# Optimization experiments

Hardware: AMD Instinct MI355X
Metric: run time of the kernel (lower is better)

Reference implementation:

```python
import jax, jax.numpy as jnp
import numpy as np


def _gru_cell(h, x, Wih, Whh, bih, bhh):
    # PyTorch GRU cell, gate order (r, z, n)
    gi = x @ Wih.T + bih      # [B, 3H]
    gh = h @ Whh.T + bhh      # [B, 3H]
    i_r, i_z, i_n = jnp.split(gi, 3, axis=-1)
    h_r, h_z, h_n = jnp.split(gh, 3, axis=-1)
    r = jax.nn.sigmoid(i_r + h_r)
    z = jax.nn.sigmoid(i_z + h_z)
    n = jnp.tanh(i_n + r * h_n)
    return (1.0 - z) * n + z * h


def _run_gru(xs, h0, Wih, Whh, bih, bhh):
    # xs: [T, B, E] -> (h_T [B, H], outputs [T, B, H])
    def step(h, x):
        h = _gru_cell(h, x, Wih, Whh, bih, bhh)
        return h, h
    return jax.lax.scan(step, h0, xs)


def setup_inputs() -> dict:
    key = jax.random.key(0)
    ks = jax.random.split(key, 14)
    V, E, H1, H2, W, C = 101, 512, 1024, 1024, 2048, 24

    def p(k, shape, fan):
        return jax.random.normal(k, shape, jnp.float32) / np.float32(np.sqrt(fan))

    return {
        "x": jax.random.randint(ks[0], (1, W, C), 0, V),
        "emb": p(ks[1], (V, E), E),
        "Wih1": p(ks[2], (3 * H1, E), E),
        "Whh1": p(ks[3], (3 * H1, H1), H1),
        "bih1": jnp.zeros((3 * H1,), jnp.float32),
        "bhh1": jnp.zeros((3 * H1,), jnp.float32),
        "Wih2f": p(ks[4], (3 * H2, H1), H1),
        "Whh2f": p(ks[5], (3 * H2, H2), H2),
        "bih2f": jnp.zeros((3 * H2,), jnp.float32),
        "bhh2f": jnp.zeros((3 * H2,), jnp.float32),
        "Wih2b": p(ks[6], (3 * H2, H1), H1),
        "Whh2b": p(ks[7], (3 * H2, H2), H2),
        "bih2b": jnp.zeros((3 * H2,), jnp.float32),
        "bhh2b": jnp.zeros((3 * H2,), jnp.float32),
    }


def reference(x, emb, Wih1, Whh1, bih1, bhh1,
              Wih2f, Whh2f, bih2f, bhh2f,
              Wih2b, Whh2b, bih2b, bhh2b):
    # x: [1, W, C] int indices. Dropout is treated as eval-mode (identity).
    Wn = x.shape[1]
    H1 = Whh1.shape[1]
    H2 = Whh2f.shape[1]

    e = emb[x[0]]                       # [W, C, E]
    xs = jnp.transpose(e, (1, 0, 2))    # [C, W, E] -- words batched together
    h0 = jnp.zeros((Wn, H1), e.dtype)
    word_emb, _ = _run_gru(xs, h0, Wih1, Whh1, bih1, bhh1)  # final hidden == last output

    # word-level bidirectional GRU, batch size 1 (the sentence)
    ws = word_emb[:, None, :]           # [W, 1, H1]
    h0w = jnp.zeros((1, H2), e.dtype)
    _, fwd = _run_gru(ws, h0w, Wih2f, Whh2f, bih2f, bhh2f)          # [W, 1, H2]
    _, bwd = _run_gru(ws[::-1], h0w, Wih2b, Whh2b, bih2b, bhh2b)    # reversed
    ctx = jnp.concatenate([fwd[:, 0, :], bwd[::-1][:, 0, :]], axis=-1)  # [W, 2*H2]

    return word_emb[None], ctx[None]    # ([1, W, H1], [1, W, 2*H2])
```

## Files before the change

### kernel.cpp

```cpp
#include <hip/hip_runtime.h>

typedef unsigned short u16;
typedef unsigned int   u32;
typedef unsigned long long u64;
typedef long long      i64;
typedef __attribute__((ext_vector_type(8))) short  short8;
typedef __attribute__((ext_vector_type(8))) __bf16 bf16x8;
typedef __attribute__((ext_vector_type(4))) float  f32x4;

#define W_N   2048
#define C_N   24
#define E_N   512
#define H_N   1024
#define G3_N  3072
#define CH    256
#define SEG   512
#define NBLK  64
#define COLS  16

#define MD_BF16 0u
#define MD_F32  1u
#define MD_ZERO 2u

__device__ inline float bf2f(u16 u) { union { u32 i; float f; } v; v.i = ((u32)u) << 16; return v.f; }
__device__ inline u16 f2bf(float f) {
  union { float f; u32 i; } v; v.f = f;
  u32 i = v.i;
  u32 r = (i + 0x7fffu + ((i >> 16) & 1u)) >> 16;
  return (u16)r;
}
__device__ inline float ld1(const void* p, size_t eoff, u32 md) {
  if (md == MD_F32) return ((const float*)p)[eoff];
  if (md == MD_ZERO) return 0.f;
  return bf2f(((const u16*)p)[eoff]);
}
__device__ inline short8 ld8(const void* p, size_t eoff, u32 md) {
  short8 r;
  if (md == MD_BF16) return *(const short8*)((const u16*)p + eoff);
  if (md == MD_ZERO) {
#pragma unroll
    for (int i = 0; i < 8; ++i) r[i] = 0;
    return r;
  }
  const float* f = (const float*)p + eoff;
#pragma unroll
  for (int i = 0; i < 8; ++i) r[i] = (short)f2bf(f[i]);
  return r;
}

__device__ inline void split8(f32x4 v0, f32x4 v1, bf16x8& hi, bf16x8& lo) {
#pragma unroll
  for (int i = 0; i < 4; ++i) {
    float f = v0[i];
    __bf16 h = (__bf16)f;
    hi[i] = h;
    lo[i] = (__bf16)(f - (float)h);
  }
#pragma unroll
  for (int i = 0; i < 4; ++i) {
    float f = v1[i];
    __bf16 h = (__bf16)f;
    hi[4 + i] = h;
    lo[4 + i] = (__bf16)(f - (float)h);
  }
}

__device__ inline void ldsplit(const void* p, size_t eoff, u32 md,
                               bf16x8& hi, bf16x8& lo) {
  if (md == MD_F32) {
    const float* f = (const float*)p + eoff;
    f32x4 v0 = *(const f32x4*)f;
    f32x4 v1 = *(const f32x4*)(f + 4);
    split8(v0, v1, hi, lo);
  } else if (md == MD_BF16) {
    union { short8 s; bf16x8 b; } u;
    u.s = *(const short8*)((const u16*)p + eoff);
    hi = u.b;
#pragma unroll
    for (int i = 0; i < 8; ++i) lo[i] = (__bf16)0.f;
  } else {
#pragma unroll
    for (int i = 0; i < 8; ++i) { hi[i] = (__bf16)0.f; lo[i] = (__bf16)0.f; }
  }
}

struct PtrPack { const void* p[14]; };

__global__ void sniffall_kernel(PtrPack pk, u32* __restrict__ flags) {
  if (threadIdx.x != 0) return;
  const int b = blockIdx.x;
  if (b == 0) {
    const int* xi = (const int*)pk.p[0];
    int oddzero = 0;
    for (int i = 0; i < 128; ++i)
      if (xi[2 * i + 1] == 0) oddzero++;
    flags[0] = (oddzero >= 120) ? 1u : 0u;
  } else {
    const u16* t = (const u16*)pk.p[b];
    int cnt = 0, nz = 0;
    for (int i = 0; i < 512; ++i) {
      u32 v = t[i];
      if (v != 0u) nz++;
      u32 e = (v >> 7) & 0xffu;
      if (e >= 100u && e <= 130u) cnt++;
    }
    flags[b] = (nz == 0) ? MD_ZERO : ((cnt >= 440) ? MD_BF16 : MD_F32);
  }
}

#define SWZ(row, kc) (((row) << 6) + ((kc) ^ (((row) & 7) << 3)))

template<int GATHER>
__global__ __launch_bounds__(256)
void mgemm_kernel(const void* __restrict__ A, const void* __restrict__ Wt,
                  const void* __restrict__ bias, float* __restrict__ Cout,
                  const void* __restrict__ X, int xoff, int gstride, int K,
                  const u32* __restrict__ flags, int afi, int wfi, int bfi,
                  int m_base) {
  __shared__ u16 AhS[64 * 64], AlS[64 * 64], BhS[64 * 64], BlS[64 * 64];
  __shared__ int arowS[64];
  const u32 am = (afi == -1) ? MD_BF16 : ((afi == -2) ? MD_F32 : flags[afi]);
  const u32 wm = flags[wfi];
  const u32 bm = flags[bfi];
  const int tid = threadIdx.x;
  const int bn0 = blockIdx.x * 64, bm0 = blockIdx.y * 64;
  if (GATHER) {
    if (tid < 64) {
      const int ar = m_base + bm0 + tid;
      int ix = flags[0] ? (int)((const i64*)X)[(size_t)ar * gstride + xoff]
                        : ((const int*)X)[(size_t)ar * gstride + xoff];
      arowS[tid] = min(max(ix, 0), 100);
    }
    __syncthreads();
  }
  const int wave = tid >> 6, lane = tid & 63;
  const int wr = (wave >> 1) * 32, wc = (wave & 1) * 32;
  const bool loA = (am == MD_F32), loB = (wm == MD_F32);

  f32x4 acc[2][2];
#pragma unroll
  for (int i = 0; i < 2; ++i)
#pragma unroll
    for (int j = 0; j < 2; ++j)
#pragma unroll
      for (int r = 0; r < 4; ++r) acc[i][j][r] = 0.f;

  for (int k0 = 0; k0 < K; k0 += 64) {
#pragma unroll
    for (int i = 0; i < 2; ++i) {
      const int ch = tid + i * 256;
      const int row = ch >> 3, kc = (ch & 7) * 8;
      {
        const int grow = GATHER ? arowS[row] : (m_base + bm0 + row);
        bf16x8 hi, lo;
        ldsplit(A, (size_t)grow * K + k0 + kc, am, hi, lo);
        const int o = SWZ(row, kc);
        *(bf16x8*)&AhS[o] = hi;
        *(bf16x8*)&AlS[o] = lo;
      }
      {
        bf16x8 hi, lo;
        ldsplit(Wt, (size_t)(bn0 + row) * K + k0 + kc, wm, hi, lo);
        const int o = SWZ(row, kc);
        *(bf16x8*)&BhS[o] = hi;
        *(bf16x8*)&BlS[o] = lo;
      }
    }
    __syncthreads();
#pragma unroll
    for (int ks = 0; ks < 64; ks += 32) {
      bf16x8 ah[2], al[2], bh[2], bl[2];
      const int lr = lane & 15, lk = ks + (lane >> 4) * 8;
#pragma unroll
      for (int i = 0; i < 2; ++i) {
        ah[i] = *(const bf16x8*)&AhS[SWZ(wr + i * 16 + lr, lk)];
        al[i] = *(const bf16x8*)&AlS[SWZ(wr + i * 16 + lr, lk)];
        bh[i] = *(const bf16x8*)&BhS[SWZ(wc + i * 16 + lr, lk)];
        bl[i] = *(const bf16x8*)&BlS[SWZ(wc + i * 16 + lr, lk)];
      }
#pragma unroll
      for (int i = 0; i < 2; ++i)
#pragma unroll
        for (int j = 0; j < 2; ++j) {
          acc[i][j] = __builtin_amdgcn_mfma_f32_16x16x32_bf16(ah[i], bh[j], acc[i][j], 0, 0, 0);
          if (loA)
            acc[i][j] = __builtin_amdgcn_mfma_f32_16x16x32_bf16(al[i], bh[j], acc[i][j], 0, 0, 0);
          if (loB)
            acc[i][j] = __builtin_amdgcn_mfma_f32_16x16x32_bf16(ah[i], bl[j], acc[i][j], 0, 0, 0);
        }
    }
    __syncthreads();
  }
  const int lr = lane & 15, m4 = (lane >> 4) * 4;
#pragma unroll
  for (int j = 0; j < 2; ++j) {
    const int n = bn0 + wc + j * 16 + lr;
    const float bv = ld1(bias, n, bm);
#pragma unroll
    for (int i = 0; i < 2; ++i) {
      const int m = bm0 + wr + i * 16 + m4;
#pragma unroll
      for (int r = 0; r < 4; ++r)
        Cout[(size_t)(m + r) * G3_N + n] = acc[i][j][r] + bv;
    }
  }
}

__device__ inline void seg_pass(
    const void* __restrict__ A, u32 am, int gather, const int* arowS, int bm0,
    const void* __restrict__ Wt, u32 wm, int bn0, int K,
    int tid, int wave, int lane,
    u16* AhS, u16* AlS, u16* B0h, u16* B0l, u16* B1h, u16* B1l, u16* B2h, u16* B2l,
    f32x4 (&aR)[2][2], f32x4 (&aZ)[2][2], f32x4 (&aN)[2][2]) {
  const bool loA = (am == MD_F32), loB = (wm == MD_F32);
  u16* BhS[3] = {B0h, B1h, B2h};
  u16* BlS[3] = {B0l, B1l, B2l};
  const int wr = (wave >> 1) * 32, wc = (wave & 1) * 32;
  for (int k0 = 0; k0 < K; k0 += 64) {
    __syncthreads();
#pragma unroll
    for (int i = 0; i < 2; ++i) {
      const int ch = tid + i * 256;
      const int row = ch >> 3, kc = (ch & 7) * 8;
      const int grow = gather ? arowS[row] : (bm0 + row);
      bf16x8 hi, lo;
      ldsplit(A, (size_t)grow * K + k0 + kc, am, hi, lo);
      const int o = SWZ(row, kc);
      *(bf16x8*)&AhS[o] = hi;
      *(bf16x8*)&AlS[o] = lo;
#pragma unroll
      for (int g = 0; g < 3; ++g) {
        bf16x8 bhi, blo;
        ldsplit(Wt, (size_t)(g * 1024 + bn0 + row) * K + k0 + kc, wm, bhi, blo);
        *(bf16x8*)&BhS[g][o] = bhi;
        *(bf16x8*)&BlS[g][o] = blo;
      }
    }
    __syncthreads();
#pragma unroll
    for (int ks = 0; ks < 64; ks += 32) {
      const int lr = lane & 15, lk = ks + (lane >> 4) * 8;
      bf16x8 ah[2], al[2];
#pragma unroll
      for (int i = 0; i < 2; ++i) {
        ah[i] = *(const bf16x8*)&AhS[SWZ(wr + i * 16 + lr, lk)];
        al[i] = *(const bf16x8*)&AlS[SWZ(wr + i * 16 + lr, lk)];
      }
#pragma unroll
      for (int g = 0; g < 3; ++g) {
        bf16x8 bh[2], bl[2];
#pragma unroll
        for (int j = 0; j < 2; ++j) {
          bh[j] = *(const bf16x8*)&BhS[g][SWZ(wc + j * 16 + lr, lk)];
          bl[j] = *(const bf16x8*)&BlS[g][SWZ(wc + j * 16 + lr, lk)];
        }
        f32x4 (&acc)[2][2] = (g == 0) ? aR : (g == 1) ? aZ : aN;
#pragma unroll
        for (int i = 0; i < 2; ++i)
#pragma unroll
          for (int j = 0; j < 2; ++j) {
            acc[i][j] = __builtin_amdgcn_mfma_f32_16x16x32_bf16(ah[i], bh[j], acc[i][j], 0, 0, 0);
            if (loA)
              acc[i][j] = __builtin_amdgcn_mfma_f32_16x16x32_bf16(al[i], bh[j], acc[i][j], 0, 0, 0);
            if (loB)
              acc[i][j] = __builtin_amdgcn_mfma_f32_16x16x32_bf16(ah[i], bl[j], acc[i][j], 0, 0, 0);
          }
      }
    }
  }
}

__global__ __launch_bounds__(256)
void fgru_kernel(const void* __restrict__ emb, const void* __restrict__ Wih,
                 const void* __restrict__ bih, const void* __restrict__ Whh,
                 const void* __restrict__ bhh,
                 const float* __restrict__ hin, float* __restrict__ hout,
                 float* __restrict__ wout,
                 const void* __restrict__ X, int xoff, int gstride,
                 const u32* __restrict__ flags) {
  __shared__ u16 AhS[64 * 64], AlS[64 * 64];
  __shared__ u16 B0h[64 * 64], B0l[64 * 64];
  __shared__ u16 B1h[64 * 64], B1l[64 * 64];
  __shared__ u16 B2h[64 * 64], B2l[64 * 64];
  __shared__ int arowS[64];
  const u32 amE = flags[1], wmI = flags[2], wmH = flags[3];
  const u32 bmI = flags[4], bmH = flags[5];
  const int tid = threadIdx.x, wave = tid >> 6, lane = tid & 63;
  const int bn0 = blockIdx.x * 64;
  const int bm0 = blockIdx.y * 64;
  if (tid < 64) {
    const int ar = bm0 + tid;
    int ix = flags[0] ? (int)((const i64*)X)[(size_t)ar * gstride + xoff]
                      : ((const int*)X)[(size_t)ar * gstride + xoff];
    arowS[tid] = min(max(ix, 0), 100);
  }

  f32x4 aR[2][2], aZ[2][2], aIN[2][2], aHN[2][2];
#pragma unroll
  for (int i = 0; i < 2; ++i)
#pragma unroll
    for (int j = 0; j < 2; ++j)
#pragma unroll
      for (int r = 0; r < 4; ++r) {
        aR[i][j][r] = 0.f; aZ[i][j][r] = 0.f;
        aIN[i][j][r] = 0.f; aHN[i][j][r] = 0.f;
      }

  seg_pass(emb, amE, 1, arowS, bm0, Wih, wmI, bn0, E_N,
           tid, wave, lane, AhS, AlS, B0h, B0l, B1h, B1l, B2h, B2l, aR, aZ, aIN);
  seg_pass(hin, MD_F32, 0, arowS, bm0, Whh, wmH, bn0, H_N,
           tid, wave, lane, AhS, AlS, B0h, B0l, B1h, B1l, B2h, B2l, aR, aZ, aHN);

  const int wr = (wave >> 1) * 32, wc = (wave & 1) * 32;
  const int lr = lane & 15, m4 = (lane >> 4) * 4;
#pragma unroll
  for (int j = 0; j < 2; ++j) {
    const int n = bn0 + wc + j * 16 + lr;
    const float biR = ld1(bih, n, bmI),        bhR = ld1(bhh, n, bmH);
    const float biZ = ld1(bih, 1024 + n, bmI), bhZ = ld1(bhh, 1024 + n, bmH);
    const float biN = ld1(bih, 2048 + n, bmI), bhN = ld1(bhh, 2048 + n, bmH);
#pragma unroll
    for (int i = 0; i < 2; ++i) {
      const int m = bm0 + wr + i * 16 + m4;
#pragma unroll
      for (int r4 = 0; r4 < 4; ++r4) {
        const size_t off = (size_t)(m + r4) * H_N + n;
        const float rg = 1.f / (1.f + expf(-(aR[i][j][r4] + biR + bhR)));
        const float zg = 1.f / (1.f + expf(-(aZ[i][j][r4] + biZ + bhZ)));
        const float ng = tanhf(aIN[i][j][r4] + biN + rg * (aHN[i][j][r4] + bhN));
        const float ho = (1.f - zg) * ng + zg * hin[off];
        hout[off] = ho;
        if (wout) wout[off] = ho;
      }
    }
  }
}

__global__ __launch_bounds__(256)
void gru_cell_kernel(const float* __restrict__ gi, const float* __restrict__ gh,
                     float* __restrict__ hf, float* __restrict__ wout, int mb) {
  const int idx = blockIdx.x * 256 + threadIdx.x;
  const int m = idx >> 10, j = idx & 1023;
  const float* gim = gi + (size_t)m * G3_N;
  const float* ghm = gh + (size_t)m * G3_N;
  const float ir = gim[j], iz = gim[1024 + j], inn = gim[2048 + j];
  const float hr = ghm[j], hz = ghm[1024 + j], hn = ghm[2048 + j];
  const float r = 1.f / (1.f + expf(-(ir + hr)));
  const float z = 1.f / (1.f + expf(-(iz + hz)));
  const float n = tanhf(inn + r * hn);
  const float ho = (1.f - z) * n + z * hf[idx];
  hf[idx] = ho;
  if (wout) wout[(size_t)(mb + m) * H_N + j] = ho;
}

__global__ __launch_bounds__(256)
void seq4_kernel(const void* __restrict__ Wf, const void* __restrict__ bf_,
                 const void* __restrict__ Wb, const void* __restrict__ bb_,
                 const float* __restrict__ gif, const float* __restrict__ gib,
                 float* __restrict__ ctx, const u32* __restrict__ flags,
                 int nsteps) {
  const int dir = blockIdx.x >> 6;
  const int blk = blockIdx.x & 63;
  const void* Whh = dir ? Wb : Wf;
  const void* bhh = dir ? bb_ : bf_;
  const float* gi = dir ? gib : gif;
  const u32 wm = flags[dir ? 11 : 7], bm = flags[dir ? 13 : 9];
  const int dirofs = dir << 10;
  const int tid = threadIdx.x, wave = tid >> 6, lane = tid & 63;
  const int j0 = blk * COLS;
  const int jw = wave * 4;

  __shared__ __align__(16) u16 wsh[48 * 1024];

  for (int e = tid * 8; e < 48 * 1024; e += 256 * 8) {
    const int lr = e >> 10, col = e & 1023;
    const int g = lr >> 4, jj = lr & 15;
    *(short8*)&wsh[e] = ld8(Whh, (size_t)(g * 1024 + j0 + jj) * 1024 + col, wm);
  }
  float br = 0.f, bz = 0.f, bn = 0.f;
  if (lane < 4) {
    br = ld1(bhh, 0 * 1024 + j0 + jw + lane, bm);
    bz = ld1(bhh, 1 * 1024 + j0 + jw + lane, bm);
    bn = ld1(bhh, 2 * 1024 + j0 + jw + lane, bm);
  }
  __syncthreads();

  float hp = 0.f;
  for (int t = 0; t < nsteps; ++t) {
    const int row = dir ? (nsteps - 1 - t) : t;
    float ir = 0.f, iz = 0.f, inn = 0.f;
    if (lane < 4) {
      const float* gim = gi + (size_t)row * G3_N + (j0 + jw + lane);
      ir = gim[0]; iz = gim[1024]; inn = gim[2048];
    }
    float hreg[16];
    if (t == 0) {
#pragma unroll
      for (int i = 0; i < 16; ++i) hreg[i] = 0.f;
    } else {
      const int prow = dir ? (nsteps - t) : (t - 1);
      const u64* hsrc = (const u64*)(ctx + (size_t)prow * 2048 + dirofs);
      u64 hv[8];
      for (;;) {
        bool bad = false;
#pragma unroll
        for (int c = 0; c < 8; ++c) {
          hv[c] = __hip_atomic_load(hsrc + c * 64 + lane,
                                    __ATOMIC_RELAXED, __HIP_MEMORY_SCOPE_AGENT);
          if ((u32)hv[c] == 0xFFFFFFFFu || (u32)(hv[c] >> 32) == 0xFFFFFFFFu)
            bad = true;
        }
        if (__ballot(bad) == 0ull) break;
        __builtin_amdgcn_s_sleep(1);
      }
#pragma unroll
      for (int c = 0; c < 8; ++c) {
        union { u64 u; float f[2]; } cv; cv.u = hv[c];
        hreg[2 * c]     = cv.f[0];
        hreg[2 * c + 1] = cv.f[1];
      }
    }
    float sv[12];
#pragma unroll
    for (int g = 0; g < 3; ++g)
#pragma unroll
      for (int jj = 0; jj < 4; ++jj) {
        const u32* wrow = (const u32*)&wsh[(g * 16 + jw + jj) * 1024];
        float s = 0.f;
#pragma unroll
        for (int c = 0; c < 8; ++c) {
          const u32 u = wrow[c * 64 + lane];
          union { u32 i; float f; } lo2, hi2;
          lo2.i = u << 16; hi2.i = u & 0xffff0000u;
          s = fmaf(lo2.f, hreg[2 * c], s);
          s = fmaf(hi2.f, hreg[2 * c + 1], s);
        }
#pragma unroll
        for (int off = 32; off > 0; off >>= 1) s += __shfl_xor(s, off);
        sv[g * 4 + jj] = s;
      }
    if (lane < 4) {
      const float hr = (lane == 0 ? sv[0] : lane == 1 ? sv[1] : lane == 2 ? sv[2] : sv[3]) + br;
      const float hz = (lane == 0 ? sv[4] : lane == 1 ? sv[5] : lane == 2 ? sv[6] : sv[7]) + bz;
      const float hn = (lane == 0 ? sv[8] : lane == 1 ? sv[9] : lane == 2 ? sv[10] : sv[11]) + bn;
      const float r = 1.f / (1.f + expf(-(ir + hr)));
      const float z = 1.f / (1.f + expf(-(iz + hz)));
      const float n = tanhf(inn + r * hn);
      const float ho = (1.f - z) * n + z * hp;
      hp = ho;
      union { float f; u32 i; } v; v.f = ho;
      __hip_atomic_store((u32*)(ctx + (size_t)row * 2048) + dirofs + j0 + jw + lane,
                         v.i, __ATOMIC_RELAXED, __HIP_MEMORY_SCOPE_AGENT);
    }
  }
}

__global__ __launch_bounds__(256)
void seq_kernel(const void* __restrict__ Whh, const void* __restrict__ bhh,
                const float* __restrict__ gi, float* hb, unsigned* cnt,
                float* __restrict__ ctx, const u32* __restrict__ flags,
                int wfi, int bfi, int word_base, int rev, int dirofs) {
  const u32 wm = flags[wfi], bm = flags[bfi];
  const int blk = blockIdx.x;
  const int tid = threadIdx.x;
  const int wave = tid >> 6, lane = tid & 63;
  const int j0 = blk * 8;

  __shared__ __align__(16) u16 wsh[24 * 1024];
  __shared__ float hshf[1024];
  __shared__ float ghs[24];
  __shared__ float bhs[24];
  __shared__ float hnew[8];

  for (int e = tid * 8; e < 24 * 1024; e += 256 * 8) {
    const int lr = e >> 10, col = e & 1023;
    const int g = lr >> 3, jj = lr & 7;
    *(short8*)&wsh[e] = ld8(Whh, (size_t)(g * 1024 + j0 + jj) * 1024 + col, wm);
  }
  if (tid < 24) bhs[tid] = ld1(bhh, (tid >> 3) * 1024 + j0 + (tid & 7), bm);
  __syncthreads();

  unsigned target = 0;
  for (int t = 0; t < SEG; ++t) {
    const int row = rev ? (SEG - 1 - t) : t;
    const int wt = word_base + row;
    const u32* hsrc = (const u32*)(hb + (t & 1) * 1024);
    u32* hdst = (u32*)hshf;
    if (wave == 0) {
#pragma unroll
      for (int c = 0; c < 16; ++c)
        hdst[c * 64 + lane] = __hip_atomic_load(hsrc + c * 64 + lane,
                                                __ATOMIC_RELAXED, __HIP_MEMORY_SCOPE_AGENT);
    }
    __syncthreads();
    float hreg[16];
#pragma unroll
    for (int c = 0; c < 8; ++c) {
      const int kp = 2 * (c * 64 + lane);
      hreg[2 * c]     = hshf[kp];
      hreg[2 * c + 1] = hshf[kp + 1];
    }
#pragma unroll
    for (int q = 0; q < 6; ++q) {
      const int lr = wave * 6 + q;
      const u32* wrow = (const u32*)&wsh[lr * 1024];
      float s = 0.f;
#pragma unroll
      for (int c = 0; c < 8; ++c) {
        const u32 u = wrow[c * 64 + lane];
        union { u32 i; float f; } lo, hi;
        lo.i = u << 16; hi.i = u & 0xffff0000u;
        s = fmaf(lo.f, hreg[2 * c], s);
        s = fmaf(hi.f, hreg[2 * c + 1], s);
      }
#pragma unroll
      for (int off = 32; off > 0; off >>= 1) s += __shfl_xor(s, off);
      if (lane == 0) ghs[lr] = s;
    }
    __syncthreads();
    if (tid < 8) {
      const int jj = tid;
      const float hr = ghs[jj] + bhs[jj];
      const float hz = ghs[8 + jj] + bhs[8 + jj];
      const float hn = ghs[16 + jj] + bhs[16 + jj];
      const float* gim = gi + (size_t)row * G3_N + (j0 + jj);
      const float ir = gim[0], iz = gim[1024], inn = gim[2048];
      const float r = 1.f / (1.f + expf(-(ir + hr)));
      const float z = 1.f / (1.f + expf(-(iz + hz)));
      const float n = tanhf(inn + r * hn);
      const float hp = hshf[j0 + jj];
      const float ho = (1.f - z) * n + z * hp;
      ctx[(size_t)wt * 2048 + dirofs + j0 + jj] = ho;
      hnew[jj] = ho;
    }
    __syncthreads();
    if (tid < 8) {
      union { float f; u32 i; } v; v.f = hnew[tid];
      __hip_atomic_store((u32*)(hb + ((t + 1) & 1) * 1024) + blk * 8 + tid, v.i,
                         __ATOMIC_RELAXED, __HIP_MEMORY_SCOPE_AGENT);
    }
    target += 128;
    if (tid == 0) {
      __hip_atomic_fetch_add(cnt, 1u, __ATOMIC_RELEASE, __HIP_MEMORY_SCOPE_AGENT);
      while (__hip_atomic_load(cnt, __ATOMIC_ACQUIRE, __HIP_MEMORY_SCOPE_AGENT) < target)
        __builtin_amdgcn_s_sleep(2);
    }
    __syncthreads();
  }
}

extern "C" void kernel_launch(void* const* d_in, const int* in_sizes, int n_in,
                              void* d_out, int out_size, void* d_ws, size_t ws_size,
                              hipStream_t stream) {
  char* w = (char*)d_ws;
  u32* flags = (u32*)(w);
  float* hbuf = (float*)(w + 1024);
  const size_t GBASE = 20480;

  hipMemsetAsync(w, 0, GBASE, stream);

  PtrPack pk;
  for (int i = 0; i < 14; ++i) pk.p[i] = d_in[i];
  sniffall_kernel<<<14, 64, 0, stream>>>(pk, flags);

  float* wemb = (float*)d_out;
  float* ctx  = (float*)d_out + (size_t)W_N * H_N;

  const size_t SZ_G  = (size_t)W_N * G3_N * 4;
  const size_t SZ_HF = (size_t)W_N * H_N * 4;
  const size_t needA = GBASE + 2 * SZ_G + SZ_HF;

  if (ws_size >= needA) {
    float* G0 = (float*)(w + GBASE);
    float* G1 = (float*)(w + GBASE + SZ_G);
    float* HA = (float*)(w + GBASE + 2 * SZ_G);
    float* HB = G0;

    hipMemsetAsync(HA, 0, SZ_HF, stream);

    float* bufs[2] = {HA, HB};
    dim3 gf(H_N / 64, W_N / 64);
    for (int c = 0; c < C_N; ++c) {
      fgru_kernel<<<gf, 256, 0, stream>>>(d_in[1], d_in[2], d_in[4], d_in[3], d_in[5],
                                          bufs[c & 1], bufs[(c + 1) & 1],
                                          (c == C_N - 1) ? wemb : (float*)nullptr,
                                          d_in[0], c, C_N, flags);
    }

    dim3 g(G3_N / 64, W_N / 64);
    mgemm_kernel<0><<<g, 256, 0, stream>>>(wemb, d_in[6], d_in[8], G0,
                                           nullptr, 0, 0, H_N, flags, -2, 6, 8, 0);
    mgemm_kernel<0><<<g, 256, 0, stream>>>(wemb, d_in[10], d_in[12], G1,
                                           nullptr, 0, 0, H_N, flags, -2, 10, 12, 0);
    hipMemsetAsync(ctx, 0xFF, (size_t)W_N * 2048 * 4, stream);
    seq4_kernel<<<2 * NBLK, 256, 0, stream>>>(d_in[7], d_in[9], d_in[11], d_in[13],
                                              G0, G1, ctx, flags, W_N);
  } else {
    float* G0  = (float*)(w + GBASE);
    float* GIc = G0;
    float* GHc = G0 + (size_t)CH * G3_N;
    float* HF  = (float*)(w + GBASE + (size_t)SEG * G3_N * 4);

    dim3 g1(G3_N / 64, CH / 64);
    for (int chk = 0; chk < W_N / CH; ++chk) {
      const int mb = chk * CH;
      hipMemsetAsync(HF, 0, (size_t)CH * H_N * 4, stream);
      for (int c = 0; c < C_N; ++c) {
        mgemm_kernel<1><<<g1, 256, 0, stream>>>(d_in[1], d_in[2], d_in[4], GIc,
                                                d_in[0], c, C_N, E_N, flags, 1, 2, 4, mb);
        mgemm_kernel<0><<<g1, 256, 0, stream>>>(HF, d_in[3], d_in[5], GHc,
                                                nullptr, 0, 0, H_N, flags, -2, 3, 5, 0);
        gru_cell_kernel<<<(CH * H_N) / 256, 256, 0, stream>>>(
            GIc, GHc, HF, (c == C_N - 1) ? wemb : (float*)nullptr, mb);
      }
    }
    dim3 g2(G3_N / 64, SEG / 64);
    for (int s = 0; s < W_N / SEG; ++s) {
      mgemm_kernel<0><<<g2, 256, 0, stream>>>(wemb, d_in[6], d_in[8], G0,
                                              nullptr, 0, 0, H_N, flags, -2, 6, 8, s * SEG);
      seq_kernel<<<128, 256, 0, stream>>>(d_in[7], d_in[9], G0, hbuf,
                                          (unsigned*)(w + 64 + (0 * 4 + s) * 64),
                                          ctx, flags, 7, 9, s * SEG, 0, 0);
    }
    for (int s = W_N / SEG - 1; s >= 0; --s) {
      mgemm_kernel<0><<<g2, 256, 0, stream>>>(wemb, d_in[10], d_in[12], G0,
                                              nullptr, 0, 0, H_N, flags, -2, 10, 12, s * SEG);
      seq_kernel<<<128, 256, 0, stream>>>(d_in[11], d_in[13], G0, hbuf + 2048,
                                          (unsigned*)(w + 64 + (1 * 4 + s) * 64),
                                          ctx, flags, 11, 13, s * SEG, 1, 1024);
    }
  }
}
```

Baseline: 10.54 ms.

## Fuse input-projection GEMMs with bidirectional recurrence in one persistent kernel

Replaces the two separate input-projection GEMM launches and the sequential recurrence kernel with a single launch. The first 128 blocks run the forward/backward recurrence, and the remaining blocks compute the GEMM tiles. The backward GEMM tiles are issued in reverse row order so its early timesteps finish first. The recurrence spin-waits on sentinel values in the pre-filled gate buffers, so it can start as soon as each row is ready instead of waiting for the full GEMM. It also drops the s_sleep in the hidden-state spin loop. This risks deadlock if the GEMM blocks are not scheduled while the recurrence blocks occupy CUs, and it adds extra memsets and polling traffic.

```diff
diff --git a/kernel.cpp b/kernel.cpp
--- a/kernel.cpp
+++ b/kernel.cpp
@@ -17,6 +17,7 @@
 #define SEG   512
 #define NBLK  64
 #define COLS  16
+#define SENT  0xFFFFFFFFu
 
 #define MD_BF16 0u
 #define MD_F32  1u
@@ -353,24 +354,97 @@
   if (wout) wout[(size_t)(mb + m) * H_N + j] = ho;
 }
 
-__global__ __launch_bounds__(256)
-void seq4_kernel(const void* __restrict__ Wf, const void* __restrict__ bf_,
-                 const void* __restrict__ Wb, const void* __restrict__ bb_,
-                 const float* __restrict__ gif, const float* __restrict__ gib,
-                 float* __restrict__ ctx, const u32* __restrict__ flags,
-                 int nsteps) {
-  const int dir = blockIdx.x >> 6;
-  const int blk = blockIdx.x & 63;
-  const void* Whh = dir ? Wb : Wf;
-  const void* bhh = dir ? bb_ : bf_;
-  const float* gi = dir ? gib : gif;
-  const u32 wm = flags[dir ? 11 : 7], bm = flags[dir ? 13 : 9];
+__device__ void mgemm_body(const float* __restrict__ A, const void* __restrict__ Wt,
+                           const void* __restrict__ bias, float* __restrict__ Cout,
+                           u32 wm, u32 bm, int bm0, int bn0, char* smem, int tid) {
+  u16* AhS = (u16*)smem;
+  u16* AlS = AhS + 4096;
+  u16* BhS = AlS + 4096;
+  u16* BlS = BhS + 4096;
+  const int wave = tid >> 6, lane = tid & 63;
+  const int wr = (wave >> 1) * 32, wc = (wave & 1) * 32;
+  const bool loB = (wm == MD_F32);
+  const int K = H_N;
+
+  f32x4 acc[2][2];
+#pragma unroll
+  for (int i = 0; i < 2; ++i)
+#pragma unroll
+    for (int j = 0; j < 2; ++j)
+#pragma unroll
+      for (int r = 0; r < 4; ++r) acc[i][j][r] = 0.f;
+
+  for (int k0 = 0; k0 < K; k0 += 64) {
+#pragma unroll
+    for (int i = 0; i < 2; ++i) {
+      const int ch = tid + i * 256;
+      const int row = ch >> 3, kc = (ch & 7) * 8;
+      {
+        bf16x8 hi, lo;
+        ldsplit(A, (size_t)(bm0 + row) * K + k0 + kc, MD_F32, hi, lo);
+        const int o = SWZ(row, kc);
+        *(bf16x8*)&AhS[o] = hi;
+        *(bf16x8*)&AlS[o] = lo;
+      }
+      {
+        bf16x8 hi, lo;
+        ldsplit(Wt, (size_t)(bn0 + row) * K + k0 + kc, wm, hi, lo);
+        const int o = SWZ(row, kc);
+        *(bf16x8*)&BhS[o] = hi;
+        *(bf16x8*)&BlS[o] = lo;
+      }
+    }
+    __syncthreads();
+#pragma unroll
+    for (int ks = 0; ks < 64; ks += 32) {
+      bf16x8 ah[2], al[2], bh[2], bl[2];
+      const int lr = lane & 15, lk = ks + (lane >> 4) * 8;
+#pragma unroll
+      for (int i = 0; i < 2; ++i) {
+        ah[i] = *(const bf16x8*)&AhS[SWZ(wr + i * 16 + lr, lk)];
+        al[i] = *(const bf16x8*)&AlS[SWZ(wr + i * 16 + lr, lk)];
+        bh[i] = *(const bf16x8*)&BhS[SWZ(wc + i * 16 + lr, lk)];
+        bl[i] = *(const bf16x8*)&BlS[SWZ(wc + i * 16 + lr, lk)];
+      }
+#pragma unroll
+      for (int i = 0; i < 2; ++i)
+#pragma unroll
+        for (int j = 0; j < 2; ++j) {
+          acc[i][j] = __builtin_amdgcn_mfma_f32_16x16x32_bf16(ah[i], bh[j], acc[i][j], 0, 0, 0);
+          acc[i][j] = __builtin_amdgcn_mfma_f32_16x16x32_bf16(al[i], bh[j], acc[i][j], 0, 0, 0);
+          if (loB)
+            acc[i][j] = __builtin_amdgcn_mfma_f32_16x16x32_bf16(ah[i], bl[j], acc[i][j], 0, 0, 0);
+        }
+    }
+    __syncthreads();
+  }
+  const int lr = lane & 15, m4 = (lane >> 4) * 4;
+#pragma unroll
+  for (int j = 0; j < 2; ++j) {
+    const int n = bn0 + wc + j * 16 + lr;
+    const float bv = ld1(bias, n, bm);
+#pragma unroll
+    for (int i = 0; i < 2; ++i) {
+      const int m = bm0 + wr + i * 16 + m4;
+#pragma unroll
+      for (int r = 0; r < 4; ++r) {
+        union { float f; u32 u; } cv; cv.f = acc[i][j][r] + bv;
+        __hip_atomic_store((u32*)Cout + (size_t)(m + r) * G3_N + n, cv.u,
+                           __ATOMIC_RELAXED, __HIP_MEMORY_SCOPE_AGENT);
+      }
+    }
+  }
+}
+
+__device__ void seq_body(const void* __restrict__ Whh, const void* __restrict__ bhh,
+                         const float* __restrict__ gi, float* __restrict__ ctx,
+                         u32 wm, u32 bm, int dir, int blk, char* smem, int tid,
+                         int nsteps) {
+  u16* wsh = (u16*)smem;
   const int dirofs = dir << 10;
-  const int tid = threadIdx.x, wave = tid >> 6, lane = tid & 63;
+  const int wave = tid >> 6, lane = tid & 63;
   const int j0 = blk * COLS;
   const int jw = wave * 4;
-
-  __shared__ __align__(16) u16 wsh[48 * 1024];
 
   for (int e = tid * 8; e < 48 * 1024; e += 256 * 8) {
     const int lr = e >> 10, col = e & 1023;
@@ -388,11 +462,23 @@
   float hp = 0.f;
   for (int t = 0; t < nsteps; ++t) {
     const int row = dir ? (nsteps - 1 - t) : t;
-    float ir = 0.f, iz = 0.f, inn = 0.f;
-    if (lane < 4) {
-      const float* gim = gi + (size_t)row * G3_N + (j0 + jw + lane);
-      ir = gim[0]; iz = gim[1024]; inn = gim[2048];
-    }
+    u32 ga = 0, gb = 0, gc = 0;
+    {
+      const u32* gp = (const u32*)(gi + (size_t)row * G3_N + (j0 + jw + (lane & 3)));
+      for (;;) {
+        if (lane < 4) {
+          ga = __hip_atomic_load(gp,        __ATOMIC_RELAXED, __HIP_MEMORY_SCOPE_AGENT);
+          gb = __hip_atomic_load(gp + 1024, __ATOMIC_RELAXED, __HIP_MEMORY_SCOPE_AGENT);
+          gc = __hip_atomic_load(gp + 2048, __ATOMIC_RELAXED, __HIP_MEMORY_SCOPE_AGENT);
+        }
+        const bool bad = (lane < 4) && (ga == SENT || gb == SENT || gc == SENT);
+        if (__ballot(bad) == 0ull) break;
+      }
+    }
+    union { u32 u; float f; } c0, c1, c2;
+    c0.u = ga; c1.u = gb; c2.u = gc;
+    const float ir = c0.f, iz = c1.f, inn = c2.f;
+
     float hreg[16];
     if (t == 0) {
 #pragma unroll
@@ -407,11 +493,10 @@
         for (int c = 0; c < 8; ++c) {
           hv[c] = __hip_atomic_load(hsrc + c * 64 + lane,
                                     __ATOMIC_RELAXED, __HIP_MEMORY_SCOPE_AGENT);
-          if ((u32)hv[c] == 0xFFFFFFFFu || (u32)(hv[c] >> 32) == 0xFFFFFFFFu)
+          if ((u32)hv[c] == SENT || (u32)(hv[c] >> 32) == SENT)
             bad = true;
         }
         if (__ballot(bad) == 0ull) break;
-        __builtin_amdgcn_s_sleep(1);
       }
 #pragma unroll
       for (int c = 0; c < 8; ++c) {
@@ -451,6 +536,34 @@
       union { float f; u32 i; } v; v.f = ho;
       __hip_atomic_store((u32*)(ctx + (size_t)row * 2048) + dirofs + j0 + jw + lane,
                          v.i, __ATOMIC_RELAXED, __HIP_MEMORY_SCOPE_AGENT);
+    }
+  }
+}
+
+__global__ __launch_bounds__(256)
+void p2_kernel(const void* __restrict__ Whf, const void* __restrict__ bhf,
+               const void* __restrict__ Whb, const void* __restrict__ bhb,
+               const void* __restrict__ Wif, const void* __restrict__ bif,
+               const void* __restrict__ Wib, const void* __restrict__ bib,
+               const float* __restrict__ wemb, float* __restrict__ G0,
+               float* __restrict__ G1, float* __restrict__ ctx,
+               const u32* __restrict__ flags, int nsteps) {
+  __shared__ __align__(16) char smem[48 * 1024 * 2];
+  const int tid = threadIdx.x;
+  const int bid = blockIdx.x;
+  if (bid < 2 * NBLK) {
+    const int dir = bid >> 6, blk = bid & 63;
+    seq_body(dir ? Whb : Whf, dir ? bhb : bhf, dir ? G1 : G0, ctx,
+             flags[dir ? 11 : 7], flags[dir ? 13 : 9], dir, blk, smem, tid, nsteps);
+  } else {
+    int b = bid - 2 * NBLK;
+    if (b < 1536) {
+      const int bx = b % 48, by = b / 48;
+      mgemm_body(wemb, Wif, bif, G0, flags[6], flags[8], by * 64, bx * 64, smem, tid);
+    } else {
+      b -= 1536;
+      const int bx = b % 48, by = 31 - (b / 48);
+      mgemm_body(wemb, Wib, bib, G1, flags[10], flags[12], by * 64, bx * 64, smem, tid);
     }
   }
 }
@@ -587,14 +700,14 @@
                                           d_in[0], c, C_N, flags);
     }
 
-    dim3 g(G3_N / 64, W_N / 64);
-    mgemm_kernel<0><<<g, 256, 0, stream>>>(wemb, d_in[6], d_in[8], G0,
-                                           nullptr, 0, 0, H_N, flags, -2, 6, 8, 0);
-    mgemm_kernel<0><<<g, 256, 0, stream>>>(wemb, d_in[10], d_in[12], G1,
-                                           nullptr, 0, 0, H_N, flags, -2, 10, 12, 0);
+    hipMemsetAsync(G0, 0xFF, SZ_G, stream);
+    hipMemsetAsync(G1, 0xFF, SZ_G, stream);
     hipMemsetAsync(ctx, 0xFF, (size_t)W_N * 2048 * 4, stream);
-    seq4_kernel<<<2 * NBLK, 256, 0, stream>>>(d_in[7], d_in[9], d_in[11], d_in[13],
-                                              G0, G1, ctx, flags, W_N);
+
+    p2_kernel<<<2 * NBLK + 2 * 1536, 256, 0, stream>>>(
+        d_in[7], d_in[9], d_in[11], d_in[13],
+        d_in[6], d_in[8], d_in[10], d_in[12],
+        wemb, G0, G1, ctx, flags, W_N);
   } else {
     float* G0  = (float*)(w + GBASE);
     float* GIc = G0;
```

Result: faster. 9.880 ms (-6.3%).
